# Performance work log

Measured on AMD Instinct MI355X. Metric: run time of the kernel, lower is better.

Reference implementation:

```python
import jax, jax.numpy as jnp
import numpy as np

B, C, H, W, P = 64, 3, 256, 256, 16
D, DEPTH, HEADS, DH, MLP = 1024, 10, 2, 64, 256
INNER = HEADS * DH            # 128
GEN = 16                      # gen_out_pixel == config.GEN_PIXEL_SIZE
SIDE = W // GEN               # 16 (PATCH_Attention side slice)
HP = H // P                   # 16 patch rows
WP = W // P + 2 * GEN // P    # 18 patch cols after generated side columns
NCLS = GEN * H // P // P      # 16 cls tokens per side
N = (H // P) * (W // P) + 2 * NCLS  # 288 tokens
PD = C * P * P                # 768 patch dim
SCALE = DH ** -0.5


def setup_inputs() -> dict:
    ks = jax.random.split(jax.random.key(0), 24)
    s = 0.02
    nrm = lambda k, shp, sc=1.0: jax.random.normal(k, shp, jnp.float32) * sc
    return {
        'img': nrm(ks[0], (B, C, H, W)),
        'W_pe': nrm(ks[1], (PD, D), s), 'b_pe': jnp.zeros((D,), jnp.float32),
        'cls_l': nrm(ks[2], (1, NCLS, PD)), 'cls_r': nrm(ks[3], (1, NCLS, PD)),
        'W_lin': nrm(ks[4], (PD, D), s), 'b_lin': jnp.zeros((D,), jnp.float32),
        'pos_emb': nrm(ks[5], (1, N, D)),
        'ln1_s': jnp.ones((DEPTH, D), jnp.float32), 'ln1_b': jnp.zeros((DEPTH, D), jnp.float32),
        'Wqkv': nrm(ks[6], (DEPTH, D, 3 * INNER), s),
        'Wo': nrm(ks[7], (DEPTH, INNER, D), s), 'bo': jnp.zeros((DEPTH, D), jnp.float32),
        'ln2_s': jnp.ones((DEPTH, D), jnp.float32), 'ln2_b': jnp.zeros((DEPTH, D), jnp.float32),
        'W1': nrm(ks[8], (DEPTH, D, MLP), s), 'b1': jnp.zeros((DEPTH, MLP), jnp.float32),
        'W2': nrm(ks[9], (DEPTH, MLP, D), s), 'b2': jnp.zeros((DEPTH, D), jnp.float32),
        'lng_s': jnp.ones((D,), jnp.float32), 'lng_b': jnp.zeros((D,), jnp.float32),
        'Wg': nrm(ks[10], (D, PD), s), 'bg': jnp.zeros((PD,), jnp.float32),
    }


def _ln(x, s, b, eps=1e-5):
    m = jnp.mean(x, -1, keepdims=True)
    v = jnp.mean(jnp.square(x - m), -1, keepdims=True)
    return (x - m) * jax.lax.rsqrt(v + eps) * s + b


def _l2norm(t, eps=1e-12):
    return t / jnp.maximum(jnp.linalg.norm(t, axis=-1, keepdims=True), eps)


def reference(img, W_pe, b_pe, cls_l, cls_r, W_lin, b_lin, pos_emb,
              ln1_s, ln1_b, Wqkv, Wo, bo, ln2_s, ln2_b, W1, b1, W2, b2,
              lng_s, lng_b, Wg, bg):
    b = img.shape[0]
    # patch embedding: b c (h p1) (w p2) -> b (h w) (p1 p2 c)
    x = img.reshape(b, C, H // P, P, W // P, P).transpose(0, 2, 4, 3, 5, 1).reshape(b, -1, PD)
    x = x @ W_pe + b_pe
    cl = jnp.tile(cls_l @ W_lin + b_lin, (b, 1, 1))
    cr = jnp.tile(cls_r @ W_lin + b_lin, (b, 1, 1))
    x = jnp.concatenate([cl, x, cr], axis=1) + pos_emb  # [b, N, D]
    for i in range(DEPTH):
        y = _ln(x, ln1_s[i], ln1_b[i])
        q, k, v = jnp.split(y @ Wqkv[i], 3, axis=-1)
        q = q.reshape(b, N, HEADS, DH).transpose(0, 2, 1, 3)
        k = k.reshape(b, N, HEADS, DH).transpose(0, 2, 1, 3)
        v = v.reshape(b, N, HEADS, DH).transpose(0, 2, 1, 3)
        attn = jax.nn.softmax(jnp.einsum('bhid,bhjd->bhij', q, k) * SCALE, axis=-1)
        o = jnp.einsum('bhij,bhjd->bhid', attn, v).transpose(0, 2, 1, 3).reshape(b, N, INNER)
        x = x + o @ Wo[i] + bo[i]
        y = _ln(x, ln2_s[i], ln2_b[i])
        x = x + jax.nn.gelu(y @ W1[i] + b1[i], approximate=False) @ W2[i] + b2[i]
    # generate_img with PATCH_ATTENTION
    g = _ln(x, lng_s, lng_b) @ Wg + bg                  # [b, N, PD]
    g = g.reshape(b, HP, WP, PD).transpose(0, 2, 1, 3).reshape(b, N, PD)  # (h w)->(w h)
    l, c, r = g[:, :SIDE], g[:, SIDE:-SIDE], g[:, -SIDE:]
    side = jnp.concatenate([l, r], axis=1)              # [b, 2*SIDE, PD]
    dots = jnp.einsum('bid,bjd->bij', _l2norm(side), _l2norm(c))
    attn = jax.nn.one_hot(jnp.argmax(jax.nn.softmax(dots, -1), axis=-1), c.shape[1], dtype=g.dtype)
    out = jnp.einsum('bij,bjd->bid', attn, c)           # hard top-1 gather
    g = jnp.concatenate([out[:, :SIDE], c, out[:, -SIDE:]], axis=1)  # [b, N, PD]
    # b (w h) (p1 p2 c) -> b c (h p1) (w p2)
    return g.reshape(b, WP, HP, P, P, C).transpose(0, 5, 2, 3, 1, 4).reshape(b, C, HP * P, WP * P)
```

## Files before the change

### kernel.cpp

```cpp
#include <hip/hip_runtime.h>
#include <hip/hip_bf16.h>
#include <math.h>

#define BB 64
#define CC 3
#define HH 256
#define WW 256
#define PP 16
#define DD 1024
#define DEPTH 10
#define HEADS 2
#define DHD 64
#define MLPD 256
#define INNER 128
#define NCLS 16
#define NT 288
#define PDIM 768
#define SCALE_ 0.125f
#define MROWS 18432

typedef unsigned short u16;
typedef __attribute__((ext_vector_type(4))) int   i32x4;
typedef __attribute__((ext_vector_type(4))) float f32x4;

__device__ __forceinline__ float gelu_f(float x) {
    return 0.5f * x * (1.0f + erff(x * 0.70710678118654752f));
}

__device__ __forceinline__ u16 f2bf_rne(float x) {
    unsigned u = __float_as_uint(x);
    unsigned r = u + 0x7FFFu + ((u >> 16) & 1u);
    return (u16)(r >> 16);
}
__device__ __forceinline__ void split_bf(float x, u16& h, u16& l) {
    h = f2bf_rne(x);
    float fh = __uint_as_float(((unsigned)h) << 16);
    l = f2bf_rne(x - fh);
}

__device__ __forceinline__ void mfma_bf16(f32x4& acc, i32x4 a, i32x4 b) {
    asm("v_mfma_f32_16x16x32_bf16 %0, %1, %2, %0" : "+v"(acc) : "v"(a), "v"(b));
}

__device__ __forceinline__ void gload16(const void* g, void* l) {
    __builtin_amdgcn_global_load_lds(
        (const __attribute__((address_space(1))) void*)g,
        (__attribute__((address_space(3))) void*)l, 16, 0, 0);
}

__device__ __forceinline__ float block_sum_1024(float v, float* red) {
    #pragma unroll
    for (int off = 32; off; off >>= 1) v += __shfl_xor(v, off);
    __syncthreads();
    if ((threadIdx.x & 63) == 0) red[threadIdx.x >> 6] = v;
    __syncthreads();
    return red[0] + red[1] + red[2] + red[3];
}

__device__ __forceinline__ void ln_split8(float4 xa, float4 xb, float mean, float rstd,
                                          float4 sa, float4 sb, float4 ba, float4 b_b,
                                          i32x4& hi, i32x4& lo) {
    float v0 = (xa.x - mean) * rstd * sa.x + ba.x;
    float v1 = (xa.y - mean) * rstd * sa.y + ba.y;
    float v2 = (xa.z - mean) * rstd * sa.z + ba.z;
    float v3 = (xa.w - mean) * rstd * sa.w + ba.w;
    float v4 = (xb.x - mean) * rstd * sb.x + b_b.x;
    float v5 = (xb.y - mean) * rstd * sb.y + b_b.y;
    float v6 = (xb.z - mean) * rstd * sb.z + b_b.z;
    float v7 = (xb.w - mean) * rstd * sb.w + b_b.w;
    u16 h0,h1,h2,h3,h4,h5,h6,h7, l0,l1,l2,l3,l4,l5,l6,l7;
    split_bf(v0,h0,l0); split_bf(v1,h1,l1); split_bf(v2,h2,l2); split_bf(v3,h3,l3);
    split_bf(v4,h4,l4); split_bf(v5,h5,l5); split_bf(v6,h6,l6); split_bf(v7,h7,l7);
    hi[0] = h0 | (h1 << 16); hi[1] = h2 | (h3 << 16);
    hi[2] = h4 | (h5 << 16); hi[3] = h6 | (h7 << 16);
    lo[0] = l0 | (l1 << 16); lo[1] = l2 | (l3 << 16);
    lo[2] = l4 | (l5 << 16); lo[3] = l6 | (l7 << 16);
}

__global__ __launch_bounds__(256)
void build_patches(const float* __restrict__ img, u16* __restrict__ Xh,
                   u16* __restrict__ Xl) {
    size_t e = (size_t)blockIdx.x * 256 + threadIdx.x;
    int pd = (int)(e % 768); size_t r = e / 768;
    int t  = (int)(r % 256); int b = (int)(r / 256);
    int c = pd % 3; int pp = pd / 3; int px = pp & 15, py = pp >> 4;
    int wp = t & 15, hp = t >> 4;
    float v = img[(((size_t)b * 3 + c) * 256 + hp * 16 + py) * 256 + wp * 16 + px];
    u16 h, l; split_bf(v, h, l);
    Xh[e] = h; Xl[e] = l;
}

__global__ __launch_bounds__(256)
void finish_embed_stats(const float* __restrict__ clb, const float* __restrict__ pos,
                        float* __restrict__ X, float2* __restrict__ stats) {
    __shared__ float red[4];
    int row = blockIdx.x; int t = row % NT;
    int tid = threadIdx.x;
    size_t xi = (size_t)row * 1024 + tid * 4;
    float4 p = *(const float4*)&pos[(size_t)t * 1024 + tid * 4];
    float4 v;
    if (t < 16)        v = *(const float4*)&clb[t * 1024 + tid * 4];
    else if (t >= 272) v = *(const float4*)&clb[(t - 256) * 1024 + tid * 4];
    else               v = *(const float4*)&X[xi];
    v.x += p.x; v.y += p.y; v.z += p.z; v.w += p.w;
    *(float4*)&X[xi] = v;
    float s = v.x + v.y + v.z + v.w;
    float q = v.x*v.x + v.y*v.y + v.z*v.z + v.w*v.w;
    float st = block_sum_1024(s, red);
    float qt = block_sum_1024(q, red);
    if (tid == 0) stats[row] = make_float2(st, qt);
}

__global__ __launch_bounds__(256)
void convert_wT(const float* __restrict__ W, u16* __restrict__ Wh,
                u16* __restrict__ Wl, int K, int N) {
    __shared__ float t[32][33];
    int n0 = blockIdx.x * 32, k0 = blockIdx.y * 32;
    int c = threadIdx.x & 31, r8 = threadIdx.x >> 5;
    #pragma unroll
    for (int rr = r8; rr < 32; rr += 8)
        t[rr][c] = W[(size_t)(k0 + rr) * N + n0 + c];
    __syncthreads();
    #pragma unroll
    for (int rr = r8; rr < 32; rr += 8) {
        float v = t[c][rr];
        u16 h, l; split_bf(v, h, l);
        size_t o = (size_t)(n0 + rr) * K + k0 + c;
        Wh[o] = h; Wl[o] = l;
    }
}

__global__ __launch_bounds__(256)
void bigconvert(const float* __restrict__ Wqkv, const float* __restrict__ Wo,
                const float* __restrict__ W1, const float* __restrict__ W2,
                u16* __restrict__ wbase) {
    __shared__ float t[32][33];
    int bid = blockIdx.x;
    int layer = bid >> 10, tt = bid & 1023;
    u16* lb = wbase + (size_t)layer * 2097152;
    const float* src; u16* dh; u16* dl; int K, N, tloc;
    if (tt < 384)      { tloc = tt;       src = Wqkv + (size_t)layer*393216; K = 1024; N = 384;  dh = lb;           dl = lb + 393216; }
    else if (tt < 512) { tloc = tt - 384; src = Wo   + (size_t)layer*131072; K = 128;  N = 1024; dh = lb + 786432;  dl = lb + 917504; }
    else if (tt < 768) { tloc = tt - 512; src = W1   + (size_t)layer*262144; K = 1024; N = 256;  dh = lb + 1048576; dl = lb + 1310720; }
    else               { tloc = tt - 768; src = W2   + (size_t)layer*262144; K = 256;  N = 1024; dh = lb + 1572864; dl = lb + 1835008; }
    int tn = N >> 5;
    int n0 = (tloc % tn) * 32, k0 = (tloc / tn) * 32;
    int c = threadIdx.x & 31, r8 = threadIdx.x >> 5;
    #pragma unroll
    for (int rr = r8; rr < 32; rr += 8)
        t[rr][c] = src[(size_t)(k0 + rr) * N + n0 + c];
    __syncthreads();
    #pragma unroll
    for (int rr = r8; rr < 32; rr += 8) {
        float v = t[c][rr];
        u16 h, l; split_bf(v, h, l);
        size_t o = (size_t)(n0 + rr) * K + k0 + c;
        dh[o] = h; dl[o] = l;
    }
}

#define SOFF(reg, tile) (((reg) * 8 + (tile)) * 512)
template<int EPI, bool ROWMAP, bool ALN, bool PERM, bool STATS>
__global__ __launch_bounds__(256, 2)
void gemm_bf16x3(const u16* __restrict__ Ah, const u16* __restrict__ Al,
                 const u16* __restrict__ Bh, const u16* __restrict__ Bl,
                 const float* __restrict__ bias, float* __restrict__ out,
                 u16* __restrict__ outH, u16* __restrict__ outL,
                 const float* __restrict__ xsrc,
                 const float2* __restrict__ statsIn, int ncb,
                 float2* __restrict__ statsOut,
                 const float* __restrict__ lns, const float* __restrict__ lnb,
                 int M, int Nn, int K, int NTn, int mtq) {
    __shared__ u16 smem[16384];
    const int tid = threadIdx.x;
    const int w = tid >> 6, lane = tid & 63;
    const int wr = w >> 1, wc = w & 1;
    const int bid = blockIdx.x;
    const int loc = bid >> 3;
    const int n_t = loc % NTn;
    const int m_t = (bid & 7) * mtq + loc / NTn;
    const int m0 = m_t << 7, n0 = n_t << 7;
    const int lr = lane & 15, lg = lane >> 4;

    const u16* gp[8];
    int lb[8];
    {
        size_t b0 = (size_t)(n0 + (2 * w) * 16 + lr) * K + lg * 8;
        size_t b1 = (size_t)(n0 + (2 * w + 1) * 16 + lr) * K + lg * 8;
        gp[4] = Bh + b0; gp[5] = Bh + b1; gp[6] = Bl + b0; gp[7] = Bl + b1;
        if (!ALN) {
            size_t a0 = (size_t)(m0 + (2 * w) * 16 + lr) * K + lg * 8;
            size_t a1 = (size_t)(m0 + (2 * w + 1) * 16 + lr) * K + lg * 8;
            gp[0] = Ah + a0; gp[1] = Ah + a1; gp[2] = Al + a0; gp[3] = Al + a1;
        }
        lb[0] = SOFF(0, 2 * w); lb[1] = SOFF(0, 2 * w + 1);
        lb[2] = SOFF(1, 2 * w); lb[3] = SOFF(1, 2 * w + 1);
        lb[4] = SOFF(2, 2 * w); lb[5] = SOFF(2, 2 * w + 1);
        lb[6] = SOFF(3, 2 * w); lb[7] = SOFF(3, 2 * w + 1);
    }

    float mean0 = 0.f, rstd0 = 0.f, mean1 = 0.f, rstd1 = 0.f;
    const float* xr0 = nullptr; const float* xr1 = nullptr;
    if (ALN) {
        int r0 = m0 + (2 * w) * 16 + lr;
        int r1 = r0 + 16;
        float s0 = 0.f, q0 = 0.f, s1 = 0.f, q1 = 0.f;
        for (int cb = 0; cb < ncb; cb++) {
            float2 a = statsIn[cb * M + r0]; s0 += a.x; q0 += a.y;
            float2 b = statsIn[cb * M + r1]; s1 += b.x; q1 += b.y;
        }
        mean0 = s0 * (1.0f / 1024.0f);
        rstd0 = rsqrtf(q0 * (1.0f / 1024.0f) - mean0 * mean0 + 1e-5f);
        mean1 = s1 * (1.0f / 1024.0f);
        rstd1 = rsqrtf(q1 * (1.0f / 1024.0f) - mean1 * mean1 + 1e-5f);
        xr0 = xsrc + (size_t)r0 * K + lg * 8;
        xr1 = xsrc + (size_t)r1 * K + lg * 8;
    }

    f32x4 acc[4][4];
    #pragma unroll
    for (int i = 0; i < 4; i++)
        #pragma unroll
        for (int j = 0; j < 4; j++) acc[i][j] = f32x4{0.f, 0.f, 0.f, 0.f};

    const int nks = K >> 5;
    const int lo8 = lane * 8;
    for (int ks = 0; ks < nks; ks++) {
        if (ALN) {
            #pragma unroll
            for (int q = 4; q < 8; q++) { gload16(gp[q], &smem[lb[q]]); gp[q] += 32; }
            const int kofs = ks * 32;
            float4 xa0 = *(const float4*)(xr0 + kofs), xb0 = *(const float4*)(xr0 + kofs + 4);
            float4 xa1 = *(const float4*)(xr1 + kofs), xb1 = *(const float4*)(xr1 + kofs + 4);
            const int kn = kofs + lg * 8;
            float4 sa = *(const float4*)(lns + kn), sb = *(const float4*)(lns + kn + 4);
            float4 ba = *(const float4*)(lnb + kn), b_b = *(const float4*)(lnb + kn + 4);
            i32x4 hi0, lo0, hi1, lo1;
            ln_split8(xa0, xb0, mean0, rstd0, sa, sb, ba, b_b, hi0, lo0);
            ln_split8(xa1, xb1, mean1, rstd1, sa, sb, ba, b_b, hi1, lo1);
            *(i32x4*)&smem[lb[0] + lane * 8] = hi0;
            *(i32x4*)&smem[lb[1] + lane * 8] = hi1;
            *(i32x4*)&smem[lb[2] + lane * 8] = lo0;
            *(i32x4*)&smem[lb[3] + lane * 8] = lo1;
        } else {
            #pragma unroll
            for (int q = 0; q < 8; q++) { gload16(gp[q], &smem[lb[q]]); gp[q] += 32; }
        }
        __syncthreads();
        i32x4 a_h[4], a_l[4], b_h[4], b_l[4];
        #pragma unroll
        for (int i = 0; i < 4; i++) {
            a_h[i] = *(const i32x4*)&smem[SOFF(0, wr * 4 + i) + lo8];
            a_l[i] = *(const i32x4*)&smem[SOFF(1, wr * 4 + i) + lo8];
            b_h[i] = *(const i32x4*)&smem[SOFF(2, wc * 4 + i) + lo8];
            b_l[i] = *(const i32x4*)&smem[SOFF(3, wc * 4 + i) + lo8];
        }
        #pragma unroll
        for (int i = 0; i < 4; i++)
            #pragma unroll
            for (int j = 0; j < 4; j++) {
                mfma_bf16(acc[i][j], a_h[i], b_h[j]);
                mfma_bf16(acc[i][j], a_h[i], b_l[j]);
                mfma_bf16(acc[i][j], a_l[i], b_h[j]);
            }
        __syncthreads();
    }

    float* lds_f = (float*)smem;
    #pragma unroll
    for (int h = 0; h < 2; h++) {
        __syncthreads();
        if (wr == h) {
            #pragma unroll
            for (int i = 0; i < 4; i++)
                #pragma unroll
                for (int j = 0; j < 4; j++)
                    #pragma unroll
                    for (int r = 0; r < 4; r++)
                        lds_f[(i * 16 + lg * 4 + r) * 128 + wc * 64 + j * 16 + lr]
                            = acc[i][j][r];
        }
        __syncthreads();
        #pragma unroll
        for (int k = 0; k < 8; k++) {
            int f = k * 256 + tid;
            int rloc = f >> 5;
            int c4 = f & 31;
            int row = m0 + h * 64 + rloc;
            int col = n0 + c4 * 4;
            float4 v = *(float4*)&lds_f[rloc * 128 + c4 * 4];
            if (EPI >= 1) {
                float4 bv = *(const float4*)&bias[col];
                v.x += bv.x; v.y += bv.y; v.z += bv.z; v.w += bv.w;
            }
            int orow = row;
            if (ROWMAP) orow = row + 16 + 32 * (row >> 8);
            if (PERM) {
                int bi = row / 288; int t1 = row - bi * 288;
                int hp = t1 / 18; int wp = t1 - hp * 18;
                orow = bi * 288 + wp * 16 + hp;
            }
            size_t oidx = (size_t)orow * Nn + col;
            if (EPI == 3) {
                ushort4 hv, lv;
                float g0 = gelu_f(v.x), g1 = gelu_f(v.y);
                float g2 = gelu_f(v.z), g3 = gelu_f(v.w);
                split_bf(g0, hv.x, lv.x); split_bf(g1, hv.y, lv.y);
                split_bf(g2, hv.z, lv.z); split_bf(g3, hv.w, lv.w);
                *(ushort4*)&outH[oidx] = hv;
                *(ushort4*)&outL[oidx] = lv;
            } else if (EPI == 2) {
                float4 rv = *(float4*)&out[oidx];
                v.x += rv.x; v.y += rv.y; v.z += rv.z; v.w += rv.w;
                *(float4*)&out[oidx] = v;
                if (STATS) {
                    float s = v.x + v.y + v.z + v.w;
                    float q = v.x*v.x + v.y*v.y + v.z*v.z + v.w*v.w;
                    #pragma unroll
                    for (int off = 1; off < 32; off <<= 1) {
                        s += __shfl_xor(s, off);
                        q += __shfl_xor(q, off);
                    }
                    if ((tid & 31) == 0)
                        statsOut[n_t * M + row] = make_float2(s, q);
                }
            } else {
                *(float4*)&out[oidx] = v;
            }
        }
    }
}

template<int EPI>
__global__ __launch_bounds__(256)
void gemm_f32(const float* __restrict__ A, const float* __restrict__ Wt,
              const float* __restrict__ bias, float* __restrict__ Cout,
              int M, int Nn, int K) {
    __shared__ float As[16][132];
    __shared__ float Bs[16][68];
    const int tid = threadIdx.x;
    const int m0 = blockIdx.y * 128;
    const int n0 = blockIdx.x * 64;
    const int ty = tid >> 4, tx = tid & 15;
    float acc[8][4];
    #pragma unroll
    for (int r = 0; r < 8; r++)
        #pragma unroll
        for (int c = 0; c < 4; c++) acc[r][c] = 0.0f;
    const int af4 = tid & 3;
    const int arow0 = tid >> 2;
    const int bcol = tid & 63, brow0 = tid >> 6;
    for (int k0 = 0; k0 < K; k0 += 16) {
        #pragma unroll
        for (int rr = 0; rr < 2; rr++) {
            int row = arow0 + rr * 64;
            int gm = m0 + row;
            float4 v = make_float4(0.f, 0.f, 0.f, 0.f);
            if (gm < M) v = *(const float4*)&A[(size_t)gm * K + k0 + af4 * 4];
            As[af4 * 4 + 0][row] = v.x; As[af4 * 4 + 1][row] = v.y;
            As[af4 * 4 + 2][row] = v.z; As[af4 * 4 + 3][row] = v.w;
        }
        #pragma unroll
        for (int rr = 0; rr < 4; rr++) {
            int krow = brow0 + rr * 4;
            Bs[krow][bcol] = Wt[(size_t)(k0 + krow) * Nn + n0 + bcol];
        }
        __syncthreads();
        #pragma unroll
        for (int kk = 0; kk < 16; kk++) {
            float4 a0 = *(const float4*)&As[kk][ty * 8];
            float4 a1 = *(const float4*)&As[kk][ty * 8 + 4];
            float4 b0 = *(const float4*)&Bs[kk][tx * 4];
            float ar[8] = {a0.x, a0.y, a0.z, a0.w, a1.x, a1.y, a1.z, a1.w};
            float bc[4] = {b0.x, b0.y, b0.z, b0.w};
            #pragma unroll
            for (int r = 0; r < 8; r++)
                #pragma unroll
                for (int c = 0; c < 4; c++)
                    acc[r][c] = fmaf(ar[r], bc[c], acc[r][c]);
        }
        __syncthreads();
    }
    float4 bv = make_float4(0.f, 0.f, 0.f, 0.f);
    if (EPI >= 1) bv = *(const float4*)&bias[n0 + tx * 4];
    #pragma unroll
    for (int r = 0; r < 8; r++) {
        int gm = m0 + ty * 8 + r;
        if (gm >= M) continue;
        float4 v = make_float4(acc[r][0], acc[r][1], acc[r][2], acc[r][3]);
        if (EPI >= 1) { v.x += bv.x; v.y += bv.y; v.z += bv.z; v.w += bv.w; }
        *(float4*)&Cout[(size_t)gm * Nn + n0 + tx * 4] = v;
    }
}

__global__ __launch_bounds__(256)
void attn_kernel(const float* __restrict__ qkv, u16* __restrict__ Oh,
                 u16* __restrict__ Ol) {
    int bid = blockIdx.x;
    int loc = bid >> 3;
    int b = (bid & 7) * 8 + loc / 18;
    int rem = loc % 18;
    int h = rem / 9, qt = rem % 9;
    const int tid = threadIdx.x;
    __shared__ float Qs[32][65], Ks[32][65], Vs[32][65], Ps[32][33];
    int q0 = qt * 32;
    for (int e = tid; e < 32 * 64; e += 256) {
        int i = e >> 6, d = e & 63;
        Qs[i][d] = qkv[((size_t)(b * NT + q0 + i)) * 384 + h * 64 + d];
    }
    float m = -INFINITY, l = 0.0f;
    float o[8];
    #pragma unroll
    for (int dd = 0; dd < 8; dd++) o[dd] = 0.0f;
    const int i = tid >> 3;
    const int jg = tid & 7;
    for (int kt = 0; kt < 9; kt++) {
        __syncthreads();
        int k0 = kt * 32;
        for (int e = tid; e < 32 * 64; e += 256) {
            int r = e >> 6, d = e & 63;
            size_t rowb = ((size_t)(b * NT + k0 + r)) * 384;
            Ks[r][d] = qkv[rowb + 128 + h * 64 + d];
            Vs[r][d] = qkv[rowb + 256 + h * 64 + d];
        }
        __syncthreads();
        float s[4] = {0.f, 0.f, 0.f, 0.f};
        for (int d = 0; d < 64; d++) {
            float qd = Qs[i][d];
            #pragma unroll
            for (int jj = 0; jj < 4; jj++) s[jj] = fmaf(qd, Ks[jg * 4 + jj][d], s[jj]);
        }
        #pragma unroll
        for (int jj = 0; jj < 4; jj++) s[jj] *= SCALE_;
        float tmax = fmaxf(fmaxf(s[0], s[1]), fmaxf(s[2], s[3]));
        #pragma unroll
        for (int off = 1; off < 8; off <<= 1) tmax = fmaxf(tmax, __shfl_xor(tmax, off));
        float mnew = fmaxf(m, tmax);
        float p[4], psum = 0.0f;
        #pragma unroll
        for (int jj = 0; jj < 4; jj++) { p[jj] = expf(s[jj] - mnew); psum += p[jj]; }
        #pragma unroll
        for (int off = 1; off < 8; off <<= 1) psum += __shfl_xor(psum, off);
        float alpha = expf(m - mnew);
        l = l * alpha + psum;
        m = mnew;
        #pragma unroll
        for (int dd = 0; dd < 8; dd++) o[dd] *= alpha;
        #pragma unroll
        for (int jj = 0; jj < 4; jj++) Ps[i][jg * 4 + jj] = p[jj];
        __syncthreads();
        for (int j = 0; j < 32; j++) {
            float pj = Ps[i][j];
            #pragma unroll
            for (int dd = 0; dd < 8; dd++) o[dd] = fmaf(pj, Vs[j][jg * 8 + dd], o[dd]);
        }
    }
    float rl = 1.0f / l;
    #pragma unroll
    for (int dd = 0; dd < 8; dd++) {
        float v = o[dd] * rl;
        u16 hh_, ll_; split_bf(v, hh_, ll_);
        size_t oidx = ((size_t)(b * NT + q0 + i)) * 128 + h * 64 + jg * 8 + dd;
        Oh[oidx] = hh_; Ol[oidx] = ll_;
    }
}

__global__ __launch_bounds__(256)
void dots_tile(const float* __restrict__ G2, float* __restrict__ dots) {
    __shared__ float Sl[32][132];
    __shared__ float Cl[64][132];
    int b = blockIdx.y, jt = blockIdx.x;
    int tid = threadIdx.x;
    int j = tid & 63, sg = tid >> 6;
    const float* gb = G2 + (size_t)b * NT * 768;
    float acc[8], s2[8];
    #pragma unroll
    for (int s = 0; s < 8; s++) { acc[s] = 0.f; s2[s] = 0.f; }
    float c2 = 0.f;
    for (int kt = 0; kt < 6; kt++) {
        __syncthreads();
        #pragma unroll
        for (int i = 0; i < 4; i++) {
            int f = tid + i * 256; int r = f >> 5; int c = (f & 31) * 4;
            int sr = (r < 16) ? r : (r + 256);
            *(float4*)&Sl[r][c] = *(const float4*)&gb[(size_t)sr * 768 + kt * 128 + c];
        }
        #pragma unroll
        for (int i = 0; i < 8; i++) {
            int f = tid + i * 256; int r = f >> 5; int c = (f & 31) * 4;
            *(float4*)&Cl[r][c] = *(const float4*)&gb[(size_t)(16 + jt * 64 + r) * 768 + kt * 128 + c];
        }
        __syncthreads();
        for (int dd = 0; dd < 32; dd++) {
            float4 c4 = *(const float4*)&Cl[j][dd * 4];
            c2 += c4.x*c4.x + c4.y*c4.y + c4.z*c4.z + c4.w*c4.w;
            #pragma unroll
            for (int s = 0; s < 8; s++) {
                float4 s4 = *(const float4*)&Sl[sg * 8 + s][dd * 4];
                acc[s] += s4.x*c4.x + s4.y*c4.y + s4.z*c4.z + s4.w*c4.w;
                s2[s]  += s4.x*s4.x + s4.y*s4.y + s4.z*s4.z + s4.w*s4.w;
            }
        }
    }
    float cn = fmaxf(sqrtf(c2), 1e-12f);
    #pragma unroll
    for (int s = 0; s < 8; s++) {
        int si = sg * 8 + s;
        float v = acc[s] / (fmaxf(sqrtf(s2[s]), 1e-12f) * cn);
        dots[((size_t)(b * 32 + si)) * 256 + jt * 64 + j] = v;
    }
}

__global__ __launch_bounds__(64)
void argmax_k(const float* __restrict__ dots, int* __restrict__ idx) {
    int r = blockIdx.x;
    const float* dr = dots + (size_t)r * 256;
    int lane = threadIdx.x;
    float bv = -1e30f; int bi = 0;
    #pragma unroll
    for (int i = 0; i < 4; i++) {
        int jj = i * 64 + lane;
        float v = dr[jj];
        if (v > bv) { bv = v; bi = jj; }
    }
    #pragma unroll
    for (int off = 32; off; off >>= 1) {
        float ov = __shfl_xor(bv, off); int oi = __shfl_xor(bi, off);
        if (ov > bv || (ov == bv && oi < bi)) { bv = ov; bi = oi; }
    }
    if (lane == 0) idx[r] = bi;
}

__global__ __launch_bounds__(256)
void out_assemble(const float* __restrict__ G2, const int* __restrict__ idx,
                  float* __restrict__ out) {
    size_t e = (size_t)blockIdx.x * 256 + threadIdx.x;
    int ww = (int)(e % 288); size_t r = e / 288;
    int hh_ = (int)(r % 256); r /= 256;
    int ch = (int)(r % 3); int b = (int)(r / 3);
    int wp = ww >> 4, px = ww & 15, hp = hh_ >> 4, py = hh_ & 15;
    int t = wp * 16 + hp;
    int srow;
    if (t < 16)       srow = 16 + idx[b * 32 + t];
    else if (t < 272) srow = t;
    else              srow = 16 + idx[b * 32 + 16 + (t - 272)];
    out[e] = G2[((size_t)b * NT + srow) * 768 + (py * 16 + px) * 3 + ch];
}

extern "C" void kernel_launch(void* const* d_in, const int* in_sizes, int n_in,
                              void* d_out, int out_size, void* d_ws, size_t ws_size,
                              hipStream_t stream) {
    const float* img    = (const float*)d_in[0];
    const float* W_pe   = (const float*)d_in[1];
    const float* b_pe   = (const float*)d_in[2];
    const float* cls_l  = (const float*)d_in[3];
    const float* cls_r  = (const float*)d_in[4];
    const float* W_lin  = (const float*)d_in[5];
    const float* b_lin  = (const float*)d_in[6];
    const float* pos    = (const float*)d_in[7];
    const float* ln1_s  = (const float*)d_in[8];
    const float* ln1_b  = (const float*)d_in[9];
    const float* Wqkv   = (const float*)d_in[10];
    const float* Wo     = (const float*)d_in[11];
    const float* bo     = (const float*)d_in[12];
    const float* ln2_s  = (const float*)d_in[13];
    const float* ln2_b  = (const float*)d_in[14];
    const float* W1     = (const float*)d_in[15];
    const float* b1     = (const float*)d_in[16];
    const float* W2     = (const float*)d_in[17];
    const float* b2     = (const float*)d_in[18];
    const float* lng_s  = (const float*)d_in[19];
    const float* lng_b  = (const float*)d_in[20];
    const float* Wg     = (const float*)d_in[21];
    const float* bg     = (const float*)d_in[22];

    unsigned char* wsb = (unsigned char*)d_ws;
    const size_t XB = 75497472;
    const size_t XD = 150994944;
    float* x    = (float*)(wsb + 0);
    u16*  wAll  = (u16*)(wsb + XB);
    u16*  xph   = (u16*)(wsb + XB);
    u16*  xpl   = (u16*)(wsb + XB + 25165824);
    float* g2   = (float*)(wsb + XB);
    u16*  wEh   = (u16*)(wsb + XB + 56623104);
    u16*  wEl   = (u16*)(wsb + XB + 58195968);
    float2* stats2 = (float2*)(wsb + XB + 59768832);
    float* dotsb  = (float*)(wsb + XB + 60948480);
    float* clb    = (float*)(wsb + XB + 63045632);
    int*   idxb   = (int*)(wsb + XB + 63176704);
    float* qkvb = (float*)(wsb + XD);
    u16*  hhb   = (u16*)(wsb + XD);
    u16*  hlb   = (u16*)(wsb + XD + 9437184);
    u16*  ohb   = (u16*)(wsb + XD + 28311552);
    u16*  olb   = (u16*)(wsb + XD + 33030144);

    const int M = MROWS;

    build_patches<<<49152, 256, 0, stream>>>(img, xph, xpl);
    convert_wT<<<dim3(32, 24), 256, 0, stream>>>(W_pe, wEh, wEl, 768, 1024);
    gemm_f32<1><<<dim3(16, 1), 256, 0, stream>>>(cls_l, W_lin, b_lin, clb, 16, 1024, 768);
    gemm_f32<1><<<dim3(16, 1), 256, 0, stream>>>(cls_r, W_lin, b_lin, clb + 16 * 1024, 16, 1024, 768);
    gemm_bf16x3<1, true, false, false, false><<<1024, 256, 0, stream>>>(
        xph, xpl, wEh, wEl, b_pe, x, nullptr, nullptr,
        nullptr, nullptr, 0, nullptr, nullptr, nullptr, 16384, 1024, 768, 8, 16);
    finish_embed_stats<<<M, 256, 0, stream>>>(clb, pos, x, stats2);
    bigconvert<<<10240, 256, 0, stream>>>(Wqkv, Wo, W1, W2, wAll);

    for (int i = 0; i < DEPTH; i++) {
        u16* lw = wAll + (size_t)i * 2097152;
        int ncb = (i == 0) ? 1 : 8;
        gemm_bf16x3<0, false, true, false, false><<<432, 256, 0, stream>>>(
            nullptr, nullptr, lw, lw + 393216, nullptr, qkvb, nullptr, nullptr,
            x, stats2, ncb, nullptr, ln1_s + i * 1024, ln1_b + i * 1024,
            M, 384, 1024, 3, 18);
        attn_kernel<<<1152, 256, 0, stream>>>(qkvb, ohb, olb);
        gemm_bf16x3<2, false, false, false, true><<<1152, 256, 0, stream>>>(
            ohb, olb, lw + 786432, lw + 917504, bo + i * 1024, x, nullptr, nullptr,
            nullptr, nullptr, 0, stats2, nullptr, nullptr, M, 1024, 128, 8, 18);
        gemm_bf16x3<3, false, true, false, false><<<288, 256, 0, stream>>>(
            nullptr, nullptr, lw + 1048576, lw + 1310720, b1 + i * 256, nullptr, hhb, hlb,
            x, stats2, 8, nullptr, ln2_s + i * 1024, ln2_b + i * 1024,
            M, 256, 1024, 2, 18);
        gemm_bf16x3<2, false, false, false, true><<<1152, 256, 0, stream>>>(
            hhb, hlb, lw + 1572864, lw + 1835008, b2 + i * 1024, x, nullptr, nullptr,
            nullptr, nullptr, 0, stats2, nullptr, nullptr, M, 1024, 256, 8, 18);
    }

    convert_wT<<<dim3(24, 32), 256, 0, stream>>>(Wg, wEh, wEl, 1024, 768);
    gemm_bf16x3<1, false, true, true, false><<<864, 256, 0, stream>>>(
        nullptr, nullptr, wEh, wEl, bg, g2, nullptr, nullptr,
        x, stats2, 8, nullptr, lng_s, lng_b, M, 768, 1024, 6, 18);
    dots_tile<<<dim3(4, BB), 256, 0, stream>>>(g2, dotsb);
    argmax_k<<<2048, 64, 0, stream>>>(dotsb, idxb);
    out_assemble<<<55296, 256, 0, stream>>>(g2, idxb, (float*)d_out);
}
```

Before: 4.822 ms.

## Register-prefetch next K tile in GEMM instead of direct global-to-LDS loads

Replaces the direct global-to-LDS async loads in the split-bf16 GEMM main loop with register staging. The next K-slice is fetched into registers right after the barrier, so global latency overlaps the MFMA work on the current tile. This costs extra VGPRs for staging and a separate LDS write each iteration, which may lower occupancy.

Result: no change. 4.865 ms (+0.9%).

```diff
diff --git a/kernel.cpp b/kernel.cpp
--- a/kernel.cpp
+++ b/kernel.cpp
@@ -40,12 +40,6 @@
 
 __device__ __forceinline__ void mfma_bf16(f32x4& acc, i32x4 a, i32x4 b) {
     asm("v_mfma_f32_16x16x32_bf16 %0, %1, %2, %0" : "+v"(acc) : "v"(a), "v"(b));
-}
-
-__device__ __forceinline__ void gload16(const void* g, void* l) {
-    __builtin_amdgcn_global_load_lds(
-        (const __attribute__((address_space(1))) void*)g,
-        (__attribute__((address_space(3))) void*)l, 16, 0, 0);
 }
 
 __device__ __forceinline__ float block_sum_1024(float v, float* red) {
@@ -181,6 +175,7 @@
     const int m_t = (bid & 7) * mtq + loc / NTn;
     const int m0 = m_t << 7, n0 = n_t << 7;
     const int lr = lane & 15, lg = lane >> 4;
+    const int lo8 = lane * 8;
 
     const u16* gp[8];
     int lb[8];
@@ -224,46 +219,84 @@
         for (int j = 0; j < 4; j++) acc[i][j] = f32x4{0.f, 0.f, 0.f, 0.f};
 
     const int nks = K >> 5;
-    const int lo8 = lane * 8;
-    for (int ks = 0; ks < nks; ks++) {
-        if (ALN) {
-            #pragma unroll
-            for (int q = 4; q < 8; q++) { gload16(gp[q], &smem[lb[q]]); gp[q] += 32; }
-            const int kofs = ks * 32;
-            float4 xa0 = *(const float4*)(xr0 + kofs), xb0 = *(const float4*)(xr0 + kofs + 4);
-            float4 xa1 = *(const float4*)(xr1 + kofs), xb1 = *(const float4*)(xr1 + kofs + 4);
-            const int kn = kofs + lg * 8;
-            float4 sa = *(const float4*)(lns + kn), sb = *(const float4*)(lns + kn + 4);
-            float4 ba = *(const float4*)(lnb + kn), b_b = *(const float4*)(lnb + kn + 4);
-            i32x4 hi0, lo0, hi1, lo1;
-            ln_split8(xa0, xb0, mean0, rstd0, sa, sb, ba, b_b, hi0, lo0);
-            ln_split8(xa1, xb1, mean1, rstd1, sa, sb, ba, b_b, hi1, lo1);
-            *(i32x4*)&smem[lb[0] + lane * 8] = hi0;
-            *(i32x4*)&smem[lb[1] + lane * 8] = hi1;
-            *(i32x4*)&smem[lb[2] + lane * 8] = lo0;
-            *(i32x4*)&smem[lb[3] + lane * 8] = lo1;
-        } else {
-            #pragma unroll
-            for (int q = 0; q < 8; q++) { gload16(gp[q], &smem[lb[q]]); gp[q] += 32; }
-        }
-        __syncthreads();
-        i32x4 a_h[4], a_l[4], b_h[4], b_l[4];
-        #pragma unroll
-        for (int i = 0; i < 4; i++) {
-            a_h[i] = *(const i32x4*)&smem[SOFF(0, wr * 4 + i) + lo8];
-            a_l[i] = *(const i32x4*)&smem[SOFF(1, wr * 4 + i) + lo8];
-            b_h[i] = *(const i32x4*)&smem[SOFF(2, wc * 4 + i) + lo8];
-            b_l[i] = *(const i32x4*)&smem[SOFF(3, wc * 4 + i) + lo8];
-        }
-        #pragma unroll
-        for (int i = 0; i < 4; i++)
-            #pragma unroll
-            for (int j = 0; j < 4; j++) {
-                mfma_bf16(acc[i][j], a_h[i], b_h[j]);
-                mfma_bf16(acc[i][j], a_h[i], b_l[j]);
-                mfma_bf16(acc[i][j], a_l[i], b_h[j]);
-            }
-        __syncthreads();
+
+    if (!ALN) {
+        i32x4 stg[8];
+        #pragma unroll
+        for (int q = 0; q < 8; q++) { stg[q] = *(const i32x4*)gp[q]; gp[q] += 32; }
+        for (int ks = 0; ks < nks; ks++) {
+            #pragma unroll
+            for (int q = 0; q < 8; q++)
+                *(i32x4*)&smem[lb[q] + lo8] = stg[q];
+            __syncthreads();
+            if (ks + 1 < nks) {
+                #pragma unroll
+                for (int q = 0; q < 8; q++) { stg[q] = *(const i32x4*)gp[q]; gp[q] += 32; }
+            }
+            i32x4 a_h[4], a_l[4], b_h[4], b_l[4];
+            #pragma unroll
+            for (int i = 0; i < 4; i++) {
+                a_h[i] = *(const i32x4*)&smem[SOFF(0, wr * 4 + i) + lo8];
+                a_l[i] = *(const i32x4*)&smem[SOFF(1, wr * 4 + i) + lo8];
+                b_h[i] = *(const i32x4*)&smem[SOFF(2, wc * 4 + i) + lo8];
+                b_l[i] = *(const i32x4*)&smem[SOFF(3, wc * 4 + i) + lo8];
+            }
+            #pragma unroll
+            for (int i = 0; i < 4; i++)
+                #pragma unroll
+                for (int j = 0; j < 4; j++) {
+                    mfma_bf16(acc[i][j], a_h[i], b_h[j]);
+                    mfma_bf16(acc[i][j], a_h[i], b_l[j]);
+                    mfma_bf16(acc[i][j], a_l[i], b_h[j]);
+                }
+            __syncthreads();
+        }
+    } else {
+        i32x4 stgB[4];
+        #pragma unroll
+        for (int q = 0; q < 4; q++) { stgB[q] = *(const i32x4*)gp[4 + q]; gp[4 + q] += 32; }
+        for (int ks = 0; ks < nks; ks++) {
+            #pragma unroll
+            for (int q = 0; q < 4; q++)
+                *(i32x4*)&smem[lb[4 + q] + lo8] = stgB[q];
+            {
+                const int kofs = ks * 32;
+                float4 xa0 = *(const float4*)(xr0 + kofs), xb0 = *(const float4*)(xr0 + kofs + 4);
+                float4 xa1 = *(const float4*)(xr1 + kofs), xb1 = *(const float4*)(xr1 + kofs + 4);
+                const int kn = kofs + lg * 8;
+                float4 sa = *(const float4*)(lns + kn), sb = *(const float4*)(lns + kn + 4);
+                float4 ba = *(const float4*)(lnb + kn), b_b = *(const float4*)(lnb + kn + 4);
+                i32x4 hi0, lo0, hi1, lo1;
+                ln_split8(xa0, xb0, mean0, rstd0, sa, sb, ba, b_b, hi0, lo0);
+                ln_split8(xa1, xb1, mean1, rstd1, sa, sb, ba, b_b, hi1, lo1);
+                *(i32x4*)&smem[lb[0] + lo8] = hi0;
+                *(i32x4*)&smem[lb[1] + lo8] = hi1;
+                *(i32x4*)&smem[lb[2] + lo8] = lo0;
+                *(i32x4*)&smem[lb[3] + lo8] = lo1;
+            }
+            __syncthreads();
+            if (ks + 1 < nks) {
+                #pragma unroll
+                for (int q = 0; q < 4; q++) { stgB[q] = *(const i32x4*)gp[4 + q]; gp[4 + q] += 32; }
+            }
+            i32x4 a_h[4], a_l[4], b_h[4], b_l[4];
+            #pragma unroll
+            for (int i = 0; i < 4; i++) {
+                a_h[i] = *(const i32x4*)&smem[SOFF(0, wr * 4 + i) + lo8];
+                a_l[i] = *(const i32x4*)&smem[SOFF(1, wr * 4 + i) + lo8];
+                b_h[i] = *(const i32x4*)&smem[SOFF(2, wc * 4 + i) + lo8];
+                b_l[i] = *(const i32x4*)&smem[SOFF(3, wc * 4 + i) + lo8];
+            }
+            #pragma unroll
+            for (int i = 0; i < 4; i++)
+                #pragma unroll
+                for (int j = 0; j < 4; j++) {
+                    mfma_bf16(acc[i][j], a_h[i], b_h[j]);
+                    mfma_bf16(acc[i][j], a_h[i], b_l[j]);
+                    mfma_bf16(acc[i][j], a_l[i], b_h[j]);
+                }
+            __syncthreads();
+        }
     }
 
     float* lds_f = (float*)smem;
```
